# Kernel tuning notes

Measured on AMD Instinct MI355X. Metric: run time of the kernel, lower is better.

The kernel has to match this reference:

```python
import jax, jax.numpy as jnp
import numpy as np

N_IMAGE, N_REGIONS = 128, 36
N_CAPTION, N_WORD = 128, 32
D = 1024
LAMBDA_SOFTMAX = 20.0
EPS = 1e-8
LEAKY_SLOPE = 0.1


def setup_inputs() -> dict:
    key = jax.random.key(0)
    k1, k2 = jax.random.split(key)
    images = jax.random.normal(k1, (N_IMAGE, N_REGIONS, D), dtype=jnp.float32)
    captions = jax.random.normal(k2, (N_CAPTION, N_WORD, D), dtype=jnp.float32)
    # all captions at max length so the per-caption loop vectorizes exactly
    cap_lens = jnp.full((N_CAPTION,), N_WORD, dtype=jnp.int32)
    return {"images": images, "captions": captions, "cap_lens": cap_lens}


def _l2norm(x, axis):
    return x / (jnp.linalg.norm(x, axis=axis, keepdims=True) + EPS)


def _focal_attn(raw):
    # raw: (..., S, Q) = context @ query^T, as in torch bmm(context, queryT)
    a = jax.nn.leaky_relu(raw, LEAKY_SLOPE)
    a = _l2norm(a, axis=-1)              # l2norm over queryL (dim=2 in torch)
    a = jnp.swapaxes(a, -1, -2)          # (..., Q, S)
    a = jax.nn.softmax(a * LAMBDA_SOFTMAX, axis=-1)
    # focal_equal: funcF = attn*S - sum_j attn_j ; mask where positive
    S = a.shape[-1]
    funcF = a * S - jnp.sum(a, axis=-1, keepdims=True)
    fattn = jnp.where(funcF > 0, 1.0, 0.0).astype(a.dtype)
    tmp = fattn * a
    return tmp / jnp.sum(tmp, axis=-1, keepdims=True)  # renormalized attn (..., Q, S)


def _cosine(a, b):
    # torch F.cosine_similarity semantics along last axis
    na = jnp.maximum(jnp.linalg.norm(a, axis=-1), EPS)
    nb = jnp.maximum(jnp.linalg.norm(b, axis=-1), EPS)
    return jnp.sum(a * b, axis=-1) / (na * nb)


def reference(images, captions, cap_lens):
    # images: (I, R, d); captions: (C, W, d); all cap_lens == W (vectorized loop)
    # ---- t2i: query = caption words, context = image regions ----
    raw_t2i = jnp.einsum('ird,cwd->cirw', images, captions)   # (C, I, R=S, W=Q)
    re_t2i = _focal_attn(raw_t2i)                             # (C, I, W, R)
    wctx_t2i = jnp.einsum('ciwr,ird->ciwd', re_t2i, images)   # (C, I, W, d)
    t2i = _cosine(captions[:, None, :, :], wctx_t2i).mean(axis=-1)  # (C, I)
    # ---- i2t: query = image regions, context = caption words ----
    raw_i2t = jnp.einsum('cwd,ird->ciwr', captions, images)   # (C, I, W=S, R=Q)
    re_i2t = _focal_attn(raw_i2t)                             # (C, I, R, W)
    wctx_i2t = jnp.einsum('cirw,cwd->cird', re_i2t, captions) # (C, I, R, d)
    i2t = _cosine(images[None, :, :, :], wctx_i2t).mean(axis=-1)    # (C, I)
    return (t2i + i2t).T                                      # (n_image, n_caption)
```

## Files before the change

### kernel.cpp

```cpp
#include <hip/hip_runtime.h>
#include <math.h>

#define NR 36
#define NW 32
#define DD 1024
#define EPSF 1e-8f

typedef _Float16 f16x8 __attribute__((ext_vector_type(8)));
typedef float f32x16 __attribute__((ext_vector_type(16)));
#define MFMA32(a, b, c) __builtin_amdgcn_mfma_f32_32x32x16_f16((a), (b), (c), 0, 0, 0)
#define GLD16(srcp, dstp)                                                              \
  __builtin_amdgcn_global_load_lds((const __attribute__((address_space(1))) void*)(srcp), \
                                   (__attribute__((address_space(3))) void*)(dstp), 16, 0, 0)

__device__ __forceinline__ float leakyf(float x) { return x > 0.f ? x : 0.1f * x; }

__global__ __launch_bounds__(256) void prep_kernel(
    const float* __restrict__ img, const float* __restrict__ cap,
    float* __restrict__ Gimg, float* __restrict__ Gcap,
    float* __restrict__ imgn, float* __restrict__ capn,
    _Float16* __restrict__ Ahf, _Float16* __restrict__ Alf,
    _Float16* __restrict__ Bhf, _Float16* __restrict__ Blf) {
  __shared__ float sA[2][NR][64];
  const int t = threadIdx.x;
  if (blockIdx.x < 128) {
    const int i = blockIdx.x;
    const float* A = img + (size_t)i * NR * DD;
    int ti = 0, tj = 0;
    const bool active = t < 171;
    if (active) {
      int rem = t, rl = 18;
      while (rem >= rl) { rem -= rl; ++ti; --rl; }
      tj = ti + rem;
    }
    const int a0 = 2 * ti, a1 = 2 * ti + 1, b0 = 2 * tj, b1 = 2 * tj + 1;
    const int sza = ti & 7, szb = tj & 7;
    const int kq8_1 = t / NR, r1 = t - kq8_1 * NR;
    const bool has2 = t < 32;
    const int s2 = t + 256;
    const int kq8_2 = s2 / NR, r2 = s2 - kq8_2 * NR;
    float4 p0a, p1a, p0b, p1b;
    float g00 = 0.f, g01 = 0.f, g10 = 0.f, g11 = 0.f;

    auto loadRegs = [&](int idx) {
      const int k0 = idx * 64;
      p0a = *(const float4*)(A + r1 * DD + k0 + kq8_1 * 8);
      p1a = *(const float4*)(A + r1 * DD + k0 + kq8_1 * 8 + 4);
      if (has2) {
        p0b = *(const float4*)(A + r2 * DD + k0 + kq8_2 * 8);
        p1b = *(const float4*)(A + r2 * DD + k0 + kq8_2 * 8 + 4);
      }
    };
    auto cw = [&](int idx, int cur) {
      const int k0 = idx * 64;
      {
        const float a[8] = {p0a.x, p0a.y, p0a.z, p0a.w, p1a.x, p1a.y, p1a.z, p1a.w};
        f16x8 hv;
#pragma unroll
        for (int j = 0; j < 8; ++j) hv[j] = (_Float16)a[j];
        const int m = i * NR + r1, mt = m >> 5, ml = m & 31;
        const int kk = k0 + kq8_1 * 8;
        const size_t fo = (((size_t)mt * 128 + (kk >> 3)) * 32 + ml) * 8;
        *(f16x8*)(Ahf + fo) = hv;
        const int sw = (r1 >> 1) & 7;
        *(float4*)&sA[cur][r1][((2 * kq8_1) ^ sw) * 4] = p0a;
        *(float4*)&sA[cur][r1][((2 * kq8_1 + 1) ^ sw) * 4] = p1a;
      }
      if (has2) {
        const float a[8] = {p0b.x, p0b.y, p0b.z, p0b.w, p1b.x, p1b.y, p1b.z, p1b.w};
        f16x8 hv;
#pragma unroll
        for (int j = 0; j < 8; ++j) hv[j] = (_Float16)a[j];
        const int m = i * NR + r2, mt = m >> 5, ml = m & 31;
        const int kk = k0 + kq8_2 * 8;
        const size_t fo = (((size_t)mt * 128 + (kk >> 3)) * 32 + ml) * 8;
        *(f16x8*)(Ahf + fo) = hv;
        const int sw = (r2 >> 1) & 7;
        *(float4*)&sA[cur][r2][((2 * kq8_2) ^ sw) * 4] = p0b;
        *(float4*)&sA[cur][r2][((2 * kq8_2 + 1) ^ sw) * 4] = p1b;
      }
    };

    loadRegs(0);
    for (int idx = 0; idx < 16; ++idx) {
      const int cur = idx & 1;
      cw(idx, cur);
      if (idx < 15) loadRegs(idx + 1);
      __syncthreads();
      if (active) {
#pragma unroll
        for (int k = 0; k < 16; ++k) {
          const float4 va0 = *(const float4*)&sA[cur][a0][(k ^ sza) * 4];
          const float4 va1 = *(const float4*)&sA[cur][a1][(k ^ sza) * 4];
          const float4 vb0 = *(const float4*)&sA[cur][b0][(k ^ szb) * 4];
          const float4 vb1 = *(const float4*)&sA[cur][b1][(k ^ szb) * 4];
          g00 = fmaf(va0.x, vb0.x, g00); g00 = fmaf(va0.y, vb0.y, g00);
          g00 = fmaf(va0.z, vb0.z, g00); g00 = fmaf(va0.w, vb0.w, g00);
          g01 = fmaf(va0.x, vb1.x, g01); g01 = fmaf(va0.y, vb1.y, g01);
          g01 = fmaf(va0.z, vb1.z, g01); g01 = fmaf(va0.w, vb1.w, g01);
          g10 = fmaf(va1.x, vb0.x, g10); g10 = fmaf(va1.y, vb0.y, g10);
          g10 = fmaf(va1.z, vb0.z, g10); g10 = fmaf(va1.w, vb0.w, g10);
          g11 = fmaf(va1.x, vb1.x, g11); g11 = fmaf(va1.y, vb1.y, g11);
          g11 = fmaf(va1.z, vb1.z, g11); g11 = fmaf(va1.w, vb1.w, g11);
        }
      }
    }
    if (active) {
      float* Gi = Gimg + (size_t)i * NR * NR;
      Gi[a0 * NR + b0] = g00; Gi[b0 * NR + a0] = g00;
      Gi[a0 * NR + b1] = g01; Gi[b1 * NR + a0] = g01;
      Gi[a1 * NR + b0] = g10; Gi[b0 * NR + a1] = g10;
      Gi[a1 * NR + b1] = g11; Gi[b1 * NR + a1] = g11;
      if (ti == tj) {
        imgn[i * NR + a0] = fmaxf(sqrtf(g00), EPSF);
        imgn[i * NR + a1] = fmaxf(sqrtf(g11), EPSF);
      }
    }
  } else {
    const int cb = blockIdx.x - 128;
    const float* A = cap + (size_t)cb * NW * DD;
    int ti = 0, tj = 0;
    const bool active = t < 136;
    if (active) {
      int rem = t, rl = 16;
      while (rem >= rl) { rem -= rl; ++ti; --rl; }
      tj = ti + rem;
    }
    const int a0 = 2 * ti, a1 = 2 * ti + 1, b0 = 2 * tj, b1 = 2 * tj + 1;
    const int sza = ti & 7, szb = tj & 7;
    const int kq8_1 = t >> 5, r1 = t & 31;
    float4 p0a, p1a;
    float g00 = 0.f, g01 = 0.f, g10 = 0.f, g11 = 0.f;

    auto loadRegs = [&](int idx) {
      const int k0 = idx * 64;
      p0a = *(const float4*)(A + r1 * DD + k0 + kq8_1 * 8);
      p1a = *(const float4*)(A + r1 * DD + k0 + kq8_1 * 8 + 4);
    };
    auto cw = [&](int idx, int cur) {
      const int k0 = idx * 64;
      const float a[8] = {p0a.x, p0a.y, p0a.z, p0a.w, p1a.x, p1a.y, p1a.z, p1a.w};
      f16x8 hv;
#pragma unroll
      for (int j = 0; j < 8; ++j) hv[j] = (_Float16)a[j];
      const int kk = k0 + kq8_1 * 8;
      const size_t fo = (((size_t)cb * 128 + (kk >> 3)) * 32 + r1) * 8;
      *(f16x8*)(Bhf + fo) = hv;
      const int sw = (r1 >> 1) & 7;
      *(float4*)&sA[cur][r1][((2 * kq8_1) ^ sw) * 4] = p0a;
      *(float4*)&sA[cur][r1][((2 * kq8_1 + 1) ^ sw) * 4] = p1a;
    };

    loadRegs(0);
    for (int idx = 0; idx < 16; ++idx) {
      const int cur = idx & 1;
      cw(idx, cur);
      if (idx < 15) loadRegs(idx + 1);
      __syncthreads();
      if (active) {
#pragma unroll
        for (int k = 0; k < 16; ++k) {
          const float4 va0 = *(const float4*)&sA[cur][a0][(k ^ sza) * 4];
          const float4 va1 = *(const float4*)&sA[cur][a1][(k ^ sza) * 4];
          const float4 vb0 = *(const float4*)&sA[cur][b0][(k ^ szb) * 4];
          const float4 vb1 = *(const float4*)&sA[cur][b1][(k ^ szb) * 4];
          g00 = fmaf(va0.x, vb0.x, g00); g00 = fmaf(va0.y, vb0.y, g00);
          g00 = fmaf(va0.z, vb0.z, g00); g00 = fmaf(va0.w, vb0.w, g00);
          g01 = fmaf(va0.x, vb1.x, g01); g01 = fmaf(va0.y, vb1.y, g01);
          g01 = fmaf(va0.z, vb1.z, g01); g01 = fmaf(va0.w, vb1.w, g01);
          g10 = fmaf(va1.x, vb0.x, g10); g10 = fmaf(va1.y, vb0.y, g10);
          g10 = fmaf(va1.z, vb0.z, g10); g10 = fmaf(va1.w, vb0.w, g10);
          g11 = fmaf(va1.x, vb1.x, g11); g11 = fmaf(va1.y, vb1.y, g11);
          g11 = fmaf(va1.z, vb1.z, g11); g11 = fmaf(va1.w, vb1.w, g11);
        }
      }
    }
    if (active) {
      float* Gc = Gcap + (size_t)cb * NW * NW;
      Gc[a0 * NW + b0] = g00; Gc[b0 * NW + a0] = g00;
      Gc[a0 * NW + b1] = g01; Gc[b1 * NW + a0] = g01;
      Gc[a1 * NW + b0] = g10; Gc[b0 * NW + a1] = g10;
      Gc[a1 * NW + b1] = g11; Gc[b1 * NW + a1] = g11;
      if (ti == tj) {
        capn[cb * NW + a0] = fmaxf(sqrtf(g00), EPSF);
        capn[cb * NW + a1] = fmaxf(sqrtf(g11), EPSF);
      }
    }
  }
}

__device__ __forceinline__ void gemm_loadA(const _Float16* __restrict__ Ahf, int Mt0, int kt,
                                           int kb, int lm, f16x8 ar[2][2]) {
#pragma unroll
  for (int mt = 0; mt < 2; ++mt)
#pragma unroll
    for (int ks = 0; ks < 2; ++ks) {
      const size_t o = (((size_t)(Mt0 + mt) * 128) + kt * 4 + ks * 2 + kb) * 256 + lm * 8;
      ar[mt][ks] = *(const f16x8*)(Ahf + o);
    }
}

__global__ __launch_bounds__(256) void mfma_gemm_kernel(
    const _Float16* __restrict__ Ahf, const _Float16* __restrict__ Alf,
    const _Float16* __restrict__ Bhf, const _Float16* __restrict__ Blf, float* __restrict__ C) {
  __shared__ _Float16 sB[2][4096];
  const int bid0 = blockIdx.x;
  const int bid = (bid0 & 7) * 144 + (bid0 >> 3);
  const int yb = bid & 31, xb = bid >> 5;
  const int n0b = yb * 4;
  const int tid = threadIdx.x;
  const int wv = tid >> 6, lane = tid & 63;
  const int lm = lane & 31, kb = lane >> 5;
  const int Mt0 = xb * 4 + (wv >> 1) * 2;
  const int nb0 = (wv & 1) * 2;
  (void)Alf; (void)Blf;

  auto stageB = [&](int kt, int buf) {
#pragma unroll
    for (int u = 0; u < 2; ++u) {
      const int cpb = wv * 4 + u * 2;
      const int cp = cpb + kb;
      const int nb = cp >> 2, kq = cp & 3;
      const _Float16* src = Bhf + (((size_t)(n0b + nb) * 128 + kt * 4 + kq) * 32 + lm) * 8;
      GLD16(src, &sB[buf][cpb * 256]);
    }
  };

  f32x16 acc[2][2];
#pragma unroll
  for (int a = 0; a < 2; ++a)
#pragma unroll
    for (int b = 0; b < 2; ++b) acc[a][b] = {};
  f16x8 ar0[2][2], ar1[2][2];

  auto computeBuf = [&](const _Float16* sb, const f16x8 ar[2][2]) {
#pragma unroll
    for (int ks = 0; ks < 2; ++ks)
#pragma unroll
      for (int ntl = 0; ntl < 2; ++ntl) {
        const int nt = nb0 + ntl;
        const int co = (nt * 4 + ks * 2 + kb) * 256 + lm * 8;
        const f16x8 bh = *(const f16x8*)&sb[co];
        acc[0][ntl] = MFMA32(ar[0][ks], bh, acc[0][ntl]);
        acc[1][ntl] = MFMA32(ar[1][ks], bh, acc[1][ntl]);
      }
  };

  stageB(0, 0);
  gemm_loadA(Ahf, Mt0, 0, kb, lm, ar0);
  for (int kt2 = 0; kt2 < 16; ++kt2) {
    const int kt = kt2 * 2;
    __syncthreads();
    if (kt + 1 < 32) {
      stageB(kt + 1, 1);
      gemm_loadA(Ahf, Mt0, kt + 1, kb, lm, ar1);
    }
    computeBuf(sB[0], ar0);
    __syncthreads();
    if (kt + 2 < 32) {
      stageB(kt + 2, 0);
      gemm_loadA(Ahf, Mt0, kt + 2, kb, lm, ar0);
    }
    computeBuf(sB[1], ar1);
  }
#pragma unroll
  for (int mt = 0; mt < 2; ++mt)
#pragma unroll
    for (int ntl = 0; ntl < 2; ++ntl) {
      const int cc = n0b + nb0 + ntl;
      const f32x16 a = acc[mt][ntl];
#pragma unroll
      for (int q = 0; q < 16; ++q) {
        const int row32 = (q & 3) + 8 * (q >> 2) + 4 * kb;
        const int m = (Mt0 + mt) * 32 + row32;
        const int il = m / NR, r = m - il * NR;
        C[((size_t)il * 128 + cc) * (NR * NW) + r * NW + lm] = a[q];
      }
    }
}

#define GCP 1040
__global__ __launch_bounds__(192, 4) void fused_attn_kernel(
    const float* __restrict__ C, const float* __restrict__ Gimg, const float* __restrict__ Gcap,
    const float* __restrict__ imgn, const float* __restrict__ capn, float* __restrict__ out) {
  const int i = blockIdx.x;
  const int cg = blockIdx.y;
  const int tid = threadIdx.x;
  const int wv = tid >> 6, lane = tid & 63;
  __shared__ float sS[2][NR * 36];
  __shared__ float sGi[NR * NR];
  __shared__ float sGc[2 * GCP];
  __shared__ float sInvR[2][NR];
  __shared__ float sInvC[2][NW];
  __shared__ float sVal[72];
  __shared__ float red[2];
  if (tid < 2) red[tid] = 0.f;
  const float* Cp = C + ((size_t)i * 128 + cg * 2) * (NR * NW);
  for (int t = tid; t < 2 * 288; t += 192) {
    const int cap = t / 288, rem = t - cap * 288;
    const int r = rem >> 3, wq = rem & 7;
    const float4 v = *(const float4*)(Cp + cap * (NR * NW) + r * NW + wq * 4);
    *(float4*)&sS[cap][r * 36 + wq * 4] = v;
  }
  const float* Gi = Gimg + (size_t)i * (NR * NR);
  for (int t = tid; t < 324; t += 192) *(float4*)&sGi[t * 4] = *(const float4*)(Gi + t * 4);
  const float* Gc0 = Gcap + (size_t)(cg * 2) * (NW * NW);
  for (int t = tid; t < 512; t += 192) {
    const int cap = t >> 8, q = t & 255;
    *(float4*)&sGc[cap * GCP + q * 4] = *(const float4*)(Gc0 + cap * (NW * NW) + q * 4);
  }
  __syncthreads();
  if (tid < 64) {
    const int cap = tid >> 5, w = tid & 31;
    float c0 = 0.f, c1 = 0.f, c2 = 0.f, c3 = 0.f;
#pragma unroll
    for (int j = 0; j < NR; j += 4) {
      const float l0 = leakyf(sS[cap][(j + 0) * 36 + w]);
      const float l1 = leakyf(sS[cap][(j + 1) * 36 + w]);
      const float l2 = leakyf(sS[cap][(j + 2) * 36 + w]);
      const float l3 = leakyf(sS[cap][(j + 3) * 36 + w]);
      c0 = fmaf(l0, l0, c0); c1 = fmaf(l1, l1, c1);
      c2 = fmaf(l2, l2, c2); c3 = fmaf(l3, l3, c3);
    }
    sInvC[cap][w] = 20.f / (sqrtf((c0 + c1) + (c2 + c3)) + EPSF);
  } else if (tid < 136) {
    const int u = tid - 64;
    const int cap = u / NR, r = u - cap * NR;
    float r0 = 0.f, r1 = 0.f, r2 = 0.f, r3 = 0.f;
#pragma unroll
    for (int k = 0; k < 8; ++k) {
      const float4 v = *(const float4*)&sS[cap][r * 36 + k * 4];
      float l;
      l = leakyf(v.x); r0 = fmaf(l, l, r0);
      l = leakyf(v.y); r1 = fmaf(l, l, r1);
      l = leakyf(v.z); r2 = fmaf(l, l, r2);
      l = leakyf(v.w); r3 = fmaf(l, l, r3);
    }
    sInvR[cap][r] = 20.f / (sqrtf((r0 + r1) + (r2 + r3)) + EPSF);
  }
  __syncthreads();
  if (tid < 64) {
    const int cap = tid >> 5, w = tid & 31;
    float z[NR];
    float m0 = -1e30f, m1 = -1e30f, m2 = -1e30f, m3 = -1e30f;
#pragma unroll
    for (int j = 0; j < NR; j += 4) {
      z[j + 0] = leakyf(sS[cap][(j + 0) * 36 + w]) * sInvR[cap][j + 0]; m0 = fmaxf(m0, z[j + 0]);
      z[j + 1] = leakyf(sS[cap][(j + 1) * 36 + w]) * sInvR[cap][j + 1]; m1 = fmaxf(m1, z[j + 1]);
      z[j + 2] = leakyf(sS[cap][(j + 2) * 36 + w]) * sInvR[cap][j + 2]; m2 = fmaxf(m2, z[j + 2]);
      z[j + 3] = leakyf(sS[cap][(j + 3) * 36 + w]) * sInvR[cap][j + 3]; m3 = fmaxf(m3, z[j + 3]);
    }
    const float mz = fmaxf(fmaxf(m0, m1), fmaxf(m2, m3));
    float a0 = 0.f, a1 = 0.f, a2 = 0.f, a3 = 0.f;
#pragma unroll
    for (int j = 0; j < NR; j += 4) {
      z[j + 0] = __expf(z[j + 0] - mz); a0 += z[j + 0];
      z[j + 1] = __expf(z[j + 1] - mz); a1 += z[j + 1];
      z[j + 2] = __expf(z[j + 2] - mz); a2 += z[j + 2];
      z[j + 3] = __expf(z[j + 3] - mz); a3 += z[j + 3];
    }
    const float thr = ((a0 + a1) + (a2 + a3)) * (1.f / NR);
    float n0 = 0.f, n1 = 0.f, n2 = 0.f, n3 = 0.f;
#pragma unroll
    for (int j = 0; j < NR; j += 4) {
      z[j + 0] = (z[j + 0] > thr) ? z[j + 0] : 0.f;
      n0 = fmaf(z[j + 0], sS[cap][(j + 0) * 36 + w], n0);
      z[j + 1] = (z[j + 1] > thr) ? z[j + 1] : 0.f;
      n1 = fmaf(z[j + 1], sS[cap][(j + 1) * 36 + w], n1);
      z[j + 2] = (z[j + 2] > thr) ? z[j + 2] : 0.f;
      n2 = fmaf(z[j + 2], sS[cap][(j + 2) * 36 + w], n2);
      z[j + 3] = (z[j + 3] > thr) ? z[j + 3] : 0.f;
      n3 = fmaf(z[j + 3], sS[cap][(j + 3) * 36 + w], n3);
    }
    const float num = (n0 + n1) + (n2 + n3);
    float d0 = 0.f, d1 = 0.f, d2 = 0.f, d3 = 0.f;
#pragma unroll
    for (int j = 0; j < NR; ++j) {
      const int cj = j >> 2;
      float h0, h1, h2, h3;
      {
        const float4 g = *(const float4*)&sGi[j * 36 + cj * 4];
        const float ge[4] = {g.x, g.y, g.z, g.w};
        h0 = 0.5f * ge[j & 3] * z[j];
        h1 = 0.f; h2 = 0.f; h3 = 0.f;
#pragma unroll
        for (int e = 0; e < 4; ++e) {
          const int k = cj * 4 + e;
          if (k > j) h1 = fmaf(ge[e], z[k], h1);
        }
      }
#pragma unroll
      for (int c = 0; c < 9; ++c) {
        if (c > cj) {
          const float4 g = *(const float4*)&sGi[j * 36 + c * 4];
          h0 = fmaf(g.x, z[c * 4 + 0], h0);
          h1 = fmaf(g.y, z[c * 4 + 1], h1);
          h2 = fmaf(g.z, z[c * 4 + 2], h2);
          h3 = fmaf(g.w, z[c * 4 + 3], h3);
        }
      }
      const float h = (h0 + h1) + (h2 + h3);
      if ((j & 3) == 0) d0 = fmaf(z[j], h, d0);
      else if ((j & 3) == 1) d1 = fmaf(z[j], h, d1);
      else if ((j & 3) == 2) d2 = fmaf(z[j], h, d2);
      else d3 = fmaf(z[j], h, d3);
    }
    const float den2 = (d0 + d1) + (d2 + d3);
    const float val = num / (capn[(cg * 2 + cap) * NW + w] * sqrtf(2.f * den2) + 1e-30f);
    float contrib = val * (1.f / NW);
#pragma unroll
    for (int d = 1; d < 32; d <<= 1) contrib += __shfl_xor(contrib, d, 64);
    if ((tid & 31) == 0) atomicAdd(&red[cap], contrib);
  } else if (lane < 36) {
    const int u = (wv - 1) * 36 + lane;
    const int cap = u / NR, r = u - cap * NR;
    float z[NW];
    float m0 = -1e30f, m1 = -1e30f, m2 = -1e30f, m3 = -1e30f;
#pragma unroll
    for (int k = 0; k < 8; ++k) {
      const float4 v = *(const float4*)&sS[cap][r * 36 + k * 4];
      z[k * 4 + 0] = leakyf(v.x) * sInvC[cap][k * 4 + 0]; m0 = fmaxf(m0, z[k * 4 + 0]);
      z[k * 4 + 1] = leakyf(v.y) * sInvC[cap][k * 4 + 1]; m1 = fmaxf(m1, z[k * 4 + 1]);
      z[k * 4 + 2] = leakyf(v.z) * sInvC[cap][k * 4 + 2]; m2 = fmaxf(m2, z[k * 4 + 2]);
      z[k * 4 + 3] = leakyf(v.w) * sInvC[cap][k * 4 + 3]; m3 = fmaxf(m3, z[k * 4 + 3]);
    }
    const float mz = fmaxf(fmaxf(m0, m1), fmaxf(m2, m3));
    float a0 = 0.f, a1 = 0.f, a2 = 0.f, a3 = 0.f;
#pragma unroll
    for (int w = 0; w < NW; w += 4) {
      z[w + 0] = __expf(z[w + 0] - mz); a0 += z[w + 0];
      z[w + 1] = __expf(z[w + 1] - mz); a1 += z[w + 1];
      z[w + 2] = __expf(z[w + 2] - mz); a2 += z[w + 2];
      z[w + 3] = __expf(z[w + 3] - mz); a3 += z[w + 3];
    }
    const float thr = ((a0 + a1) + (a2 + a3)) * (1.f / NW);
    float n0 = 0.f, n1 = 0.f, n2 = 0.f, n3 = 0.f;
#pragma unroll
    for (int k = 0; k < 8; ++k) {
      const float4 v = *(const float4*)&sS[cap][r * 36 + k * 4];
      z[k * 4 + 0] = (z[k * 4 + 0] > thr) ? z[k * 4 + 0] : 0.f;
      n0 = fmaf(z[k * 4 + 0], v.x, n0);
      z[k * 4 + 1] = (z[k * 4 + 1] > thr) ? z[k * 4 + 1] : 0.f;
      n1 = fmaf(z[k * 4 + 1], v.y, n1);
      z[k * 4 + 2] = (z[k * 4 + 2] > thr) ? z[k * 4 + 2] : 0.f;
      n2 = fmaf(z[k * 4 + 2], v.z, n2);
      z[k * 4 + 3] = (z[k * 4 + 3] > thr) ? z[k * 4 + 3] : 0.f;
      n3 = fmaf(z[k * 4 + 3], v.w, n3);
    }
    const float num = (n0 + n1) + (n2 + n3);
    const float* Gp = &sGc[cap * GCP];
    float d0 = 0.f, d1 = 0.f, d2 = 0.f, d3 = 0.f;
#pragma unroll
    for (int w = 0; w < NW; ++w) {
      const int cw = w >> 2;
      float h0, h1, h2, h3;
      {
        const float4 g = *(const float4*)&Gp[w * 32 + cw * 4];
        const float ge[4] = {g.x, g.y, g.z, g.w};
        h0 = 0.5f * ge[w & 3] * z[w];
        h1 = 0.f; h2 = 0.f; h3 = 0.f;
#pragma unroll
        for (int e = 0; e < 4; ++e) {
          const int k = cw * 4 + e;
          if (k > w) h1 = fmaf(ge[e], z[k], h1);
        }
      }
#pragma unroll
      for (int c = 0; c < 8; ++c) {
        if (c > cw) {
          const float4 g = *(const float4*)&Gp[w * 32 + c * 4];
          h0 = fmaf(g.x, z[c * 4 + 0], h0);
          h1 = fmaf(g.y, z[c * 4 + 1], h1);
          h2 = fmaf(g.z, z[c * 4 + 2], h2);
          h3 = fmaf(g.w, z[c * 4 + 3], h3);
        }
      }
      const float h = (h0 + h1) + (h2 + h3);
      if ((w & 3) == 0) d0 = fmaf(z[w], h, d0);
      else if ((w & 3) == 1) d1 = fmaf(z[w], h, d1);
      else if ((w & 3) == 2) d2 = fmaf(z[w], h, d2);
      else d3 = fmaf(z[w], h, d3);
    }
    const float den2 = (d0 + d1) + (d2 + d3);
    const float val = num / (imgn[i * NR + r] * sqrtf(2.f * den2) + 1e-30f);
    sVal[u] = val * (1.f / NR);
  }
  __syncthreads();
  if (tid < 64) {
    const int cap = tid >> 5, x = tid & 31;
    float v = sVal[cap * 36 + x];
    if (x < 4) v += sVal[cap * 36 + 32 + x];
#pragma unroll
    for (int d = 1; d < 32; d <<= 1) v += __shfl_xor(v, d, 64);
    if ((tid & 31) == 0) atomicAdd(&red[cap], v);
  }
  __syncthreads();
  if (tid < 2) out[(size_t)i * 128 + cg * 2 + tid] = red[tid];
}

extern "C" void kernel_launch(void* const* d_in, const int* in_sizes, int n_in,
                              void* d_out, int out_size, void* d_ws, size_t ws_size,
                              hipStream_t stream) {
  (void)in_sizes; (void)n_in; (void)out_size; (void)ws_size;
  const float* images = (const float*)d_in[0];
  const float* captions = (const float*)d_in[1];
  float* out = (float*)d_out;

  char* wb = (char*)d_ws;
  _Float16* Ahf = (_Float16*)wb; wb += (size_t)4608 * 1024 * 2;
  _Float16* Alf = (_Float16*)wb; wb += (size_t)4608 * 1024 * 2;
  _Float16* Bhf = (_Float16*)wb; wb += (size_t)4096 * 1024 * 2;
  _Float16* Blf = (_Float16*)wb; wb += (size_t)4096 * 1024 * 2;
  float* Gimg = (float*)wb; wb += (size_t)128 * NR * NR * 4;
  float* Gcap = (float*)wb; wb += (size_t)128 * NW * NW * 4;
  float* imgn = (float*)wb; wb += (size_t)128 * NR * 4;
  float* capn = (float*)wb; wb += (size_t)128 * NW * 4;
  float* C = (float*)wb;

  prep_kernel<<<256, 256, 0, stream>>>(images, captions, Gimg, Gcap, imgn, capn,
                                       Ahf, Alf, Bhf, Blf);
  mfma_gemm_kernel<<<1152, 256, 0, stream>>>(Ahf, Alf, Bhf, Blf, C);
  fused_attn_kernel<<<dim3(128, 64), 192, 0, stream>>>(C, Gimg, Gcap, imgn, capn, out);
}
```

Baseline: 239.8 us.

## Deepen GEMM K-staging and repad attention shared-memory tiles

```diff
diff --git a/kernel.cpp b/kernel.cpp
--- a/kernel.cpp
+++ b/kernel.cpp
@@ -203,7 +203,7 @@
 __global__ __launch_bounds__(256) void mfma_gemm_kernel(
     const _Float16* __restrict__ Ahf, const _Float16* __restrict__ Alf,
     const _Float16* __restrict__ Bhf, const _Float16* __restrict__ Blf, float* __restrict__ C) {
-  __shared__ _Float16 sB[2][4096];
+  __shared__ _Float16 sB[2][8192];
   const int bid0 = blockIdx.x;
   const int bid = (bid0 & 7) * 144 + (bid0 >> 3);
   const int yb = bid & 31, xb = bid >> 5;
@@ -215,14 +215,15 @@
   const int nb0 = (wv & 1) * 2;
   (void)Alf; (void)Blf;
 
-  auto stageB = [&](int kt, int buf) {
-#pragma unroll
-    for (int u = 0; u < 2; ++u) {
-      const int cpb = wv * 4 + u * 2;
+  auto stageB2 = [&](int p, int buf) {
+#pragma unroll
+    for (int u = 0; u < 4; ++u) {
+      const int kt = 2 * p + (u >> 1);
+      const int cpb = wv * 4 + (u & 1) * 2;
       const int cp = cpb + kb;
       const int nb = cp >> 2, kq = cp & 3;
       const _Float16* src = Bhf + (((size_t)(n0b + nb) * 128 + kt * 4 + kq) * 32 + lm) * 8;
-      GLD16(src, &sB[buf][cpb * 256]);
+      GLD16(src, &sB[buf][(u >> 1) * 4096 + cpb * 256]);
     }
   };
 
@@ -231,9 +232,13 @@
   for (int a = 0; a < 2; ++a)
 #pragma unroll
     for (int b = 0; b < 2; ++b) acc[a][b] = {};
-  f16x8 ar0[2][2], ar1[2][2];
-
-  auto computeBuf = [&](const _Float16* sb, const f16x8 ar[2][2]) {
+  f16x8 arE[2][2][2], arO[2][2][2];
+
+  auto loadA2 = [&](int p, f16x8 ar[2][2][2]) {
+#pragma unroll
+    for (int kh = 0; kh < 2; ++kh) gemm_loadA(Ahf, Mt0, 2 * p + kh, kb, lm, ar[kh]);
+  };
+  auto computeHalf = [&](const _Float16* sb, const f16x8 ar[2][2]) {
 #pragma unroll
     for (int ks = 0; ks < 2; ++ks)
 #pragma unroll
@@ -245,23 +250,25 @@
         acc[1][ntl] = MFMA32(ar[1][ks], bh, acc[1][ntl]);
       }
   };
-
-  stageB(0, 0);
-  gemm_loadA(Ahf, Mt0, 0, kb, lm, ar0);
-  for (int kt2 = 0; kt2 < 16; ++kt2) {
-    const int kt = kt2 * 2;
+  auto computeP = [&](const _Float16* sb, const f16x8 ar[2][2][2]) {
+    computeHalf(sb, ar[0]);
+    computeHalf(sb + 4096, ar[1]);
+  };
+
+  stageB2(0, 0);
+  loadA2(0, arE);
+  for (int pp = 0; pp < 8; ++pp) {
+    const int p = 2 * pp;
     __syncthreads();
-    if (kt + 1 < 32) {
-      stageB(kt + 1, 1);
-      gemm_loadA(Ahf, Mt0, kt + 1, kb, lm, ar1);
-    }
-    computeBuf(sB[0], ar0);
+    stageB2(p + 1, 1);
+    loadA2(p + 1, arO);
+    computeP(sB[0], arE);
     __syncthreads();
-    if (kt + 2 < 32) {
-      stageB(kt + 2, 0);
-      gemm_loadA(Ahf, Mt0, kt + 2, kb, lm, ar0);
-    }
-    computeBuf(sB[1], ar1);
+    if (p + 2 < 16) {
+      stageB2(p + 2, 0);
+      loadA2(p + 2, arE);
+    }
+    computeP(sB[1], arO);
   }
 #pragma unroll
   for (int mt = 0; mt < 2; ++mt)
@@ -279,17 +286,17 @@
     }
 }
 
-#define GCP 1040
-__global__ __launch_bounds__(192, 4) void fused_attn_kernel(
+#define SP 37
+__global__ __launch_bounds__(192) void fused_attn_kernel(
     const float* __restrict__ C, const float* __restrict__ Gimg, const float* __restrict__ Gcap,
     const float* __restrict__ imgn, const float* __restrict__ capn, float* __restrict__ out) {
   const int i = blockIdx.x;
   const int cg = blockIdx.y;
   const int tid = threadIdx.x;
   const int wv = tid >> 6, lane = tid & 63;
-  __shared__ float sS[2][NR * 36];
+  __shared__ float sS[2][NR * SP];
   __shared__ float sGi[NR * NR];
-  __shared__ float sGc[2 * GCP];
+  __shared__ float sGc[2][1024];
   __shared__ float sInvR[2][NR];
   __shared__ float sInvC[2][NW];
   __shared__ float sVal[72];
@@ -300,94 +307,77 @@
     const int cap = t / 288, rem = t - cap * 288;
     const int r = rem >> 3, wq = rem & 7;
     const float4 v = *(const float4*)(Cp + cap * (NR * NW) + r * NW + wq * 4);
-    *(float4*)&sS[cap][r * 36 + wq * 4] = v;
+    float* dst = &sS[cap][r * SP + wq * 4];
+    dst[0] = v.x; dst[1] = v.y; dst[2] = v.z; dst[3] = v.w;
   }
   const float* Gi = Gimg + (size_t)i * (NR * NR);
   for (int t = tid; t < 324; t += 192) *(float4*)&sGi[t * 4] = *(const float4*)(Gi + t * 4);
   const float* Gc0 = Gcap + (size_t)(cg * 2) * (NW * NW);
   for (int t = tid; t < 512; t += 192) {
     const int cap = t >> 8, q = t & 255;
-    *(float4*)&sGc[cap * GCP + q * 4] = *(const float4*)(Gc0 + cap * (NW * NW) + q * 4);
+    *(float4*)&sGc[cap][q * 4] = *(const float4*)(Gc0 + cap * (NW * NW) + q * 4);
   }
   __syncthreads();
   if (tid < 64) {
     const int cap = tid >> 5, w = tid & 31;
-    float c0 = 0.f, c1 = 0.f, c2 = 0.f, c3 = 0.f;
-#pragma unroll
-    for (int j = 0; j < NR; j += 4) {
-      const float l0 = leakyf(sS[cap][(j + 0) * 36 + w]);
-      const float l1 = leakyf(sS[cap][(j + 1) * 36 + w]);
-      const float l2 = leakyf(sS[cap][(j + 2) * 36 + w]);
-      const float l3 = leakyf(sS[cap][(j + 3) * 36 + w]);
+    float c0 = 0.f, c1 = 0.f;
+#pragma unroll
+    for (int j = 0; j < NR; j += 2) {
+      const float l0 = leakyf(sS[cap][(j + 0) * SP + w]);
+      const float l1 = leakyf(sS[cap][(j + 1) * SP + w]);
       c0 = fmaf(l0, l0, c0); c1 = fmaf(l1, l1, c1);
-      c2 = fmaf(l2, l2, c2); c3 = fmaf(l3, l3, c3);
-    }
-    sInvC[cap][w] = 20.f / (sqrtf((c0 + c1) + (c2 + c3)) + EPSF);
+    }
+    sInvC[cap][w] = 20.f / (sqrtf(c0 + c1) + EPSF);
   } else if (tid < 136) {
     const int u = tid - 64;
     const int cap = u / NR, r = u - cap * NR;
-    float r0 = 0.f, r1 = 0.f, r2 = 0.f, r3 = 0.f;
-#pragma unroll
-    for (int k = 0; k < 8; ++k) {
-      const float4 v = *(const float4*)&sS[cap][r * 36 + k * 4];
-      float l;
-      l = leakyf(v.x); r0 = fmaf(l, l, r0);
-      l = leakyf(v.y); r1 = fmaf(l, l, r1);
-      l = leakyf(v.z); r2 = fmaf(l, l, r2);
-      l = leakyf(v.w); r3 = fmaf(l, l, r3);
-    }
-    sInvR[cap][r] = 20.f / (sqrtf((r0 + r1) + (r2 + r3)) + EPSF);
+    float r0 = 0.f, r1 = 0.f;
+#pragma unroll
+    for (int w = 0; w < NW; w += 2) {
+      const float l0 = leakyf(sS[cap][r * SP + w + 0]);
+      const float l1 = leakyf(sS[cap][r * SP + w + 1]);
+      r0 = fmaf(l0, l0, r0); r1 = fmaf(l1, l1, r1);
+    }
+    sInvR[cap][r] = 20.f / (sqrtf(r0 + r1) + EPSF);
   }
   __syncthreads();
   if (tid < 64) {
     const int cap = tid >> 5, w = tid & 31;
     float z[NR];
-    float m0 = -1e30f, m1 = -1e30f, m2 = -1e30f, m3 = -1e30f;
-#pragma unroll
-    for (int j = 0; j < NR; j += 4) {
-      z[j + 0] = leakyf(sS[cap][(j + 0) * 36 + w]) * sInvR[cap][j + 0]; m0 = fmaxf(m0, z[j + 0]);
-      z[j + 1] = leakyf(sS[cap][(j + 1) * 36 + w]) * sInvR[cap][j + 1]; m1 = fmaxf(m1, z[j + 1]);
-      z[j + 2] = leakyf(sS[cap][(j + 2) * 36 + w]) * sInvR[cap][j + 2]; m2 = fmaxf(m2, z[j + 2]);
-      z[j + 3] = leakyf(sS[cap][(j + 3) * 36 + w]) * sInvR[cap][j + 3]; m3 = fmaxf(m3, z[j + 3]);
-    }
-    const float mz = fmaxf(fmaxf(m0, m1), fmaxf(m2, m3));
-    float a0 = 0.f, a1 = 0.f, a2 = 0.f, a3 = 0.f;
-#pragma unroll
-    for (int j = 0; j < NR; j += 4) {
+    float m0 = -1e30f, m1 = -1e30f;
+#pragma unroll
+    for (int j = 0; j < NR; j += 2) {
+      z[j + 0] = leakyf(sS[cap][(j + 0) * SP + w]) * sInvR[cap][j + 0]; m0 = fmaxf(m0, z[j + 0]);
+      z[j + 1] = leakyf(sS[cap][(j + 1) * SP + w]) * sInvR[cap][j + 1]; m1 = fmaxf(m1, z[j + 1]);
+    }
+    const float mz = fmaxf(m0, m1);
+    float a0 = 0.f, a1 = 0.f;
+#pragma unroll
+    for (int j = 0; j < NR; j += 2) {
       z[j + 0] = __expf(z[j + 0] - mz); a0 += z[j + 0];
       z[j + 1] = __expf(z[j + 1] - mz); a1 += z[j + 1];
-      z[j + 2] = __expf(z[j + 2] - mz); a2 += z[j + 2];
-      z[j + 3] = __expf(z[j + 3] - mz); a3 += z[j + 3];
-    }
-    const float thr = ((a0 + a1) + (a2 + a3)) * (1.f / NR);
-    float n0 = 0.f, n1 = 0.f, n2 = 0.f, n3 = 0.f;
-#pragma unroll
-    for (int j = 0; j < NR; j += 4) {
+    }
+    const float thr = (a0 + a1) * (1.f / NR);
+    float n0 = 0.f, n1 = 0.f;
+#pragma unroll
+    for (int j = 0; j < NR; j += 2) {
       z[j + 0] = (z[j + 0] > thr) ? z[j + 0] : 0.f;
-      n0 = fmaf(z[j + 0], sS[cap][(j + 0) * 36 + w], n0);
+      n0 = fmaf(z[j + 0], sS[cap][(j + 0) * SP + w], n0);
       z[j + 1] = (z[j + 1] > thr) ? z[j + 1] : 0.f;
-      n1 = fmaf(z[j + 1], sS[cap][(j + 1) * 36 + w], n1);
-      z[j + 2] = (z[j + 2] > thr) ? z[j + 2] : 0.f;
-      n2 = fmaf(z[j + 2], sS[cap][(j + 2) * 36 + w], n2);
-      z[j + 3] = (z[j + 3] > thr) ? z[j + 3] : 0.f;
-      n3 = fmaf(z[j + 3], sS[cap][(j + 3) * 36 + w], n3);
-    }
-    const float num = (n0 + n1) + (n2 + n3);
-    float d0 = 0.f, d1 = 0.f, d2 = 0.f, d3 = 0.f;
+      n1 = fmaf(z[j + 1], sS[cap][(j + 1) * SP + w], n1);
+    }
+    const float num = n0 + n1;
+    float den2 = 0.f;
 #pragma unroll
     for (int j = 0; j < NR; ++j) {
       const int cj = j >> 2;
-      float h0, h1, h2, h3;
-      {
-        const float4 g = *(const float4*)&sGi[j * 36 + cj * 4];
-        const float ge[4] = {g.x, g.y, g.z, g.w};
-        h0 = 0.5f * ge[j & 3] * z[j];
-        h1 = 0.f; h2 = 0.f; h3 = 0.f;
-#pragma unroll
-        for (int e = 0; e < 4; ++e) {
-          const int k = cj * 4 + e;
-          if (k > j) h1 = fmaf(ge[e], z[k], h1);
-        }
+      const float4 gd = *(const float4*)&sGi[j * 36 + cj * 4];
+      const float ge[4] = {gd.x, gd.y, gd.z, gd.w};
+      float h0 = 0.5f * ge[j & 3] * z[j], h1 = 0.f, h2 = 0.f, h3 = 0.f;
+#pragma unroll
+      for (int e = 0; e < 4; ++e) {
+        const int k = cj * 4 + e;
+        if (k > j) h1 = fmaf(ge[e], z[k], h1);
       }
 #pragma unroll
       for (int c = 0; c < 9; ++c) {
@@ -399,13 +389,8 @@
           h3 = fmaf(g.w, z[c * 4 + 3], h3);
         }
       }
-      const float h = (h0 + h1) + (h2 + h3);
-      if ((j & 3) == 0) d0 = fmaf(z[j], h, d0);
-      else if ((j & 3) == 1) d1 = fmaf(z[j], h, d1);
-      else if ((j & 3) == 2) d2 = fmaf(z[j], h, d2);
-      else d3 = fmaf(z[j], h, d3);
-    }
-    const float den2 = (d0 + d1) + (d2 + d3);
+      den2 = fmaf(z[j], (h0 + h1) + (h2 + h3), den2);
+    }
     const float val = num / (capn[(cg * 2 + cap) * NW + w] * sqrtf(2.f * den2) + 1e-30f);
     float contrib = val * (1.f / NW);
 #pragma unroll
@@ -415,55 +400,41 @@
     const int u = (wv - 1) * 36 + lane;
     const int cap = u / NR, r = u - cap * NR;
     float z[NW];
-    float m0 = -1e30f, m1 = -1e30f, m2 = -1e30f, m3 = -1e30f;
-#pragma unroll
-    for (int k = 0; k < 8; ++k) {
-      const float4 v = *(const float4*)&sS[cap][r * 36 + k * 4];
-      z[k * 4 + 0] = leakyf(v.x) * sInvC[cap][k * 4 + 0]; m0 = fmaxf(m0, z[k * 4 + 0]);
-      z[k * 4 + 1] = leakyf(v.y) * sInvC[cap][k * 4 + 1]; m1 = fmaxf(m1, z[k * 4 + 1]);
-      z[k * 4 + 2] = leakyf(v.z) * sInvC[cap][k * 4 + 2]; m2 = fmaxf(m2, z[k * 4 + 2]);
-      z[k * 4 + 3] = leakyf(v.w) * sInvC[cap][k * 4 + 3]; m3 = fmaxf(m3, z[k * 4 + 3]);
-    }
-    const float mz = fmaxf(fmaxf(m0, m1), fmaxf(m2, m3));
-    float a0 = 0.f, a1 = 0.f, a2 = 0.f, a3 = 0.f;
-#pragma unroll
-    for (int w = 0; w < NW; w += 4) {
+    float m0 = -1e30f, m1 = -1e30f;
+#pragma unroll
+    for (int w = 0; w < NW; w += 2) {
+      z[w + 0] = leakyf(sS[cap][r * SP + w + 0]) * sInvC[cap][w + 0]; m0 = fmaxf(m0, z[w + 0]);
+      z[w + 1] = leakyf(sS[cap][r * SP + w + 1]) * sInvC[cap][w + 1]; m1 = fmaxf(m1, z[w + 1]);
+    }
+    const float mz = fmaxf(m0, m1);
+    float a0 = 0.f, a1 = 0.f;
+#pragma unroll
+    for (int w = 0; w < NW; w += 2) {
       z[w + 0] = __expf(z[w + 0] - mz); a0 += z[w + 0];
       z[w + 1] = __expf(z[w + 1] - mz); a1 += z[w + 1];
-      z[w + 2] = __expf(z[w + 2] - mz); a2 += z[w + 2];
-      z[w + 3] = __expf(z[w + 3] - mz); a3 += z[w + 3];
-    }
-    const float thr = ((a0 + a1) + (a2 + a3)) * (1.f / NW);
-    float n0 = 0.f, n1 = 0.f, n2 = 0.f, n3 = 0.f;
-#pragma unroll
-    for (int k = 0; k < 8; ++k) {
-      const float4 v = *(const float4*)&sS[cap][r * 36 + k * 4];
-      z[k * 4 + 0] = (z[k * 4 + 0] > thr) ? z[k * 4 + 0] : 0.f;
-      n0 = fmaf(z[k * 4 + 0], v.x, n0);
-      z[k * 4 + 1] = (z[k * 4 + 1] > thr) ? z[k * 4 + 1] : 0.f;
-      n1 = fmaf(z[k * 4 + 1], v.y, n1);
-      z[k * 4 + 2] = (z[k * 4 + 2] > thr) ? z[k * 4 + 2] : 0.f;
-      n2 = fmaf(z[k * 4 + 2], v.z, n2);
-      z[k * 4 + 3] = (z[k * 4 + 3] > thr) ? z[k * 4 + 3] : 0.f;
-      n3 = fmaf(z[k * 4 + 3], v.w, n3);
-    }
-    const float num = (n0 + n1) + (n2 + n3);
-    const float* Gp = &sGc[cap * GCP];
-    float d0 = 0.f, d1 = 0.f, d2 = 0.f, d3 = 0.f;
+    }
+    const float thr = (a0 + a1) * (1.f / NW);
+    float n0 = 0.f, n1 = 0.f;
+#pragma unroll
+    for (int w = 0; w < NW; w += 2) {
+      z[w + 0] = (z[w + 0] > thr) ? z[w + 0] : 0.f;
+      n0 = fmaf(z[w + 0], sS[cap][r * SP + w + 0], n0);
+      z[w + 1] = (z[w + 1] > thr) ? z[w + 1] : 0.f;
+      n1 = fmaf(z[w + 1], sS[cap][r * SP + w + 1], n1);
+    }
+    const float num = n0 + n1;
+    const float* Gp = &sGc[cap][0];
+    float den2 = 0.f;
 #pragma unroll
     for (int w = 0; w < NW; ++w) {
       const int cw = w >> 2;
-      float h0, h1, h2, h3;
-      {
-        const float4 g = *(const float4*)&Gp[w * 32 + cw * 4];
-        const float ge[4] = {g.x, g.y, g.z, g.w};
-        h0 = 0.5f * ge[w & 3] * z[w];
-        h1 = 0.f; h2 = 0.f; h3 = 0.f;
-#pragma unroll
-        for (int e = 0; e < 4; ++e) {
-          const int k = cw * 4 + e;
-          if (k > w) h1 = fmaf(ge[e], z[k], h1);
-        }
+      const float4 gd = *(const float4*)&Gp[w * 32 + cw * 4];
+      const float ge[4] = {gd.x, gd.y, gd.z, gd.w};
+      float h0 = 0.5f * ge[w & 3] * z[w], h1 = 0.f, h2 = 0.f, h3 = 0.f;
+#pragma unroll
+      for (int e = 0; e < 4; ++e) {
+        const int k = cw * 4 + e;
+        if (k > w) h1 = fmaf(ge[e], z[k], h1);
       }
 #pragma unroll
       for (int c = 0; c < 8; ++c) {
@@ -475,13 +446,8 @@
           h3 = fmaf(g.w, z[c * 4 + 3], h3);
         }
       }
-      const float h = (h0 + h1) + (h2 + h3);
-      if ((w & 3) == 0) d0 = fmaf(z[w], h, d0);
-      else if ((w & 3) == 1) d1 = fmaf(z[w], h, d1);
-      else if ((w & 3) == 2) d2 = fmaf(z[w], h, d2);
-      else d3 = fmaf(z[w], h, d3);
-    }
-    const float den2 = (d0 + d1) + (d2 + d3);
+      den2 = fmaf(z[w], (h0 + h1) + (h2 + h3), den2);
+    }
     const float val = num / (imgn[i * NR + r] * sqrtf(2.f * den2) + 1e-30f);
     sVal[u] = val * (1.f / NR);
   }
```

New measurement: 228.7 us. 1.05x faster.
